# Kernel tuning notes

Hardware: AMD Instinct MI355X
Metric: run time of the kernel (lower is better)

## Reference

```python
import jax, jax.numpy as jnp
import numpy as np

W_WORKERS = 2
Q_LEN = 16
HIDDEN = 4096
N_HEADS = 32
N_KV = 8
HEAD_DIM = 128
L_SHARED = 8192
L_WORKER = 2048
THETA = 10000.0


def rotate_half(x):
    x1, x2 = jnp.split(x, 2, axis=-1)
    return jnp.concatenate((-x2, x1), axis=-1)


def rope_cos_sin(pos):
    # pos: int array [...]; returns cos,sin of shape [..., HEAD_DIM] (HF convention: freqs duplicated)
    inv = 1.0 / (THETA ** (jnp.arange(0, HEAD_DIM, 2, dtype=jnp.float32) / HEAD_DIM))
    ang = pos[..., None].astype(jnp.float32) * inv
    emb = jnp.concatenate((ang, ang), axis=-1)
    return jnp.cos(emb), jnp.sin(emb)


def setup_inputs() -> dict:
    key = jax.random.key(0)
    ks = jax.random.split(key, 16)
    std = 0.02
    # new keys are appended at positions L_WORKER..L_WORKER+Q-1 of each worker's own segment
    pos_new = jnp.broadcast_to(L_WORKER + jnp.arange(Q_LEN), (W_WORKERS, Q_LEN))
    cos_new, sin_new = rope_cos_sin(pos_new)
    return {
        'hidden_states': jax.random.normal(ks[0], (W_WORKERS, Q_LEN, HIDDEN), jnp.float32),
        'Wq': jax.random.normal(ks[1], (N_HEADS * HEAD_DIM, HIDDEN), jnp.float32) * std,
        'bq': jnp.zeros((N_HEADS * HEAD_DIM,), jnp.float32),
        'Wk': jax.random.normal(ks[2], (N_KV * HEAD_DIM, HIDDEN), jnp.float32) * std,
        'bk': jnp.zeros((N_KV * HEAD_DIM,), jnp.float32),
        'Wv': jax.random.normal(ks[3], (N_KV * HEAD_DIM, HIDDEN), jnp.float32) * std,
        'bv': jnp.zeros((N_KV * HEAD_DIM,), jnp.float32),
        'Wo': jax.random.normal(ks[4], (HIDDEN, N_HEADS * HEAD_DIM), jnp.float32) * std,
        'seg_shared_k': jax.random.normal(ks[5], (N_KV, L_SHARED, HEAD_DIM), jnp.float32),
        'seg_shared_v': jax.random.normal(ks[6], (N_KV, L_SHARED, HEAD_DIM), jnp.float32),
        'w0_k': jax.random.normal(ks[7], (N_KV, L_WORKER, HEAD_DIM), jnp.float32),
        'w0_v': jax.random.normal(ks[8], (N_KV, L_WORKER, HEAD_DIM), jnp.float32),
        'w1_k': jax.random.normal(ks[9], (N_KV, L_WORKER, HEAD_DIM), jnp.float32),
        'w1_v': jax.random.normal(ks[10], (N_KV, L_WORKER, HEAD_DIM), jnp.float32),
        'cos_new': cos_new,
        'sin_new': sin_new,
    }


def reference(hidden_states, Wq, bq, Wk, bk, Wv, bv, Wo,
              seg_shared_k, seg_shared_v, w0_k, w0_v, w1_k, w1_v,
              cos_new, sin_new):
    W, Q, _ = hidden_states.shape
    scale = HEAD_DIM ** -0.5
    # projections -> [W, n_heads, Q, D]
    q = (hidden_states @ Wq.T + bq).reshape(W, Q, N_HEADS, HEAD_DIM).transpose(0, 2, 1, 3)
    k_new = (hidden_states @ Wk.T + bk).reshape(W, Q, N_KV, HEAD_DIM).transpose(0, 2, 1, 3)
    v_new = (hidden_states @ Wv.T + bv).reshape(W, Q, N_KV, HEAD_DIM).transpose(0, 2, 1, 3)
    # rope new keys (unsqueeze_dim=1: broadcast over kv heads)
    c, s = cos_new[:, None], sin_new[:, None]
    k_new = k_new * c + rotate_half(k_new) * s
    # cache update: segment 0 = shared prompt, segment 1/2 = worker 0/1 own cache (grows by Q)
    keys = [seg_shared_k,
            jnp.concatenate([w0_k, k_new[0]], axis=1),
            jnp.concatenate([w1_k, k_new[1]], axis=1)]
    values = [seg_shared_v,
              jnp.concatenate([w0_v, v_new[0]], axis=1),
              jnp.concatenate([w1_v, v_new[1]], axis=1)]
    frag_lens = [L_SHARED, L_WORKER + Q, L_WORKER + Q]
    # worker w's view: [shared, other worker's cache, own cache]
    orders = [[0, 2, 1], [0, 1, 2]]
    loc = np.zeros((3, W_WORKERS, Q), dtype=np.int32)
    for w, order in enumerate(orders):
        pos = 0
        for seg in reversed(order):
            pos += frag_lens[seg]
            loc[seg, w] = np.arange(pos - Q, pos)
    loc = jnp.asarray(loc)  # [S, W, Q]
    cos_q, sin_q = rope_cos_sin(loc)  # [S, W, Q, D]
    # hogwild_rope: queries rotated per (segment, worker) location -> [S, W, H, Q, D]
    rq = q[None] * cos_q[:, :, None] + rotate_half(q)[None] * sin_q[:, :, None]
    rep = N_HEADS // N_KV
    scores, v_parts = [], []
    for seg in range(3):
        k_s = jnp.repeat(keys[seg], rep, axis=0)  # GQA expand [H, L_s, D]
        sc = jnp.einsum('whqd,hld->whql', rq[seg], k_s) * scale
        mask = jnp.arange(frag_lens[seg])[None, None, None, :] <= loc[seg][:, None, :, None]
        scores.append(jnp.where(mask, sc, jnp.finfo(sc.dtype).min))
        v_parts.append(jnp.repeat(values[seg], rep, axis=0))
    scores = jnp.concatenate(scores, axis=-1)        # [W, H, Q, Ltot] joint softmax over fragments
    probs = jax.nn.softmax(scores, axis=-1)
    v_all = jnp.concatenate(v_parts, axis=1)         # [H, Ltot, D]
    attn = jnp.einsum('whql,hld->whqd', probs, v_all)
    out = attn.transpose(0, 2, 1, 3).reshape(W, Q, N_HEADS * HEAD_DIM) @ Wo.T
    return out
```

## Files before the change

kernel.cpp:

```cpp
#include <hip/hip_runtime.h>
#include <hip/hip_fp16.h>
#include <cstdint>
#include <cstddef>

#define QL 16
#define LSH 8192
#define LWK 2048
#define SCALE 0.08838834764831845f

typedef __attribute__((ext_vector_type(8))) short short8;
typedef __attribute__((ext_vector_type(4))) short short4v;
typedef __attribute__((ext_vector_type(4))) float f32x4;
typedef __attribute__((ext_vector_type(8))) unsigned short ushort8v;

#if defined(__has_builtin)
#if __has_builtin(__builtin_amdgcn_mfma_f32_16x16x16bf16_1k)
#define HAVE_MFMA16 1
#endif
#endif

__device__ __forceinline__ unsigned short f2bf(float f) {
  unsigned int u = __float_as_uint(f);
  u += 0x7fffu + ((u >> 16) & 1u);
  return (unsigned short)(u >> 16);
}
__device__ __forceinline__ float bf2f(unsigned short b) {
  return __uint_as_float(((unsigned int)b) << 16);
}

__device__ __forceinline__ void gload_lds16(const float* g, float* lds) {
  __builtin_amdgcn_global_load_lds(
      (const __attribute__((address_space(1))) void*)g,
      (__attribute__((address_space(3))) void*)lds, 16, 0, 0);
}

__global__ __launch_bounds__(256) void k_cast(
    const float* __restrict__ in, unsigned short* __restrict__ outp, int n4)
{
  int i = blockIdx.x * 256 + threadIdx.x;
  if (i < n4) {
    float4 v = ((const float4*)in)[i];
    ushort4 p; p.x = f2bf(v.x); p.y = f2bf(v.y); p.z = f2bf(v.z); p.w = f2bf(v.w);
    ((ushort4*)outp)[i] = p;
  }
}

__global__ __launch_bounds__(256) void k_gemm4(
    const unsigned short* __restrict__ Xbf,
    const float* __restrict__ W0, const float* __restrict__ W1, const float* __restrict__ W2,
    const float* __restrict__ b0, const float* __restrict__ b1, const float* __restrict__ b2,
    float* __restrict__ outA, float* __restrict__ outB, int Ntot)
{
  __shared__ float Ws[16 * 516];
  const int bx = blockIdx.x;
  const int n0 = (bx >> 1) * 16;
  const int khalf = bx & 1;
  const float* W; const float* bias; int row0;
  if (n0 < 4096)      { W = W0; bias = b0; row0 = n0; }
  else if (n0 < 5120) { W = W1; bias = b1; row0 = n0 - 4096; }
  else                { W = W2; bias = b2; row0 = n0 - 5120; }
  const int t = threadIdx.x;
  const int w_id = t >> 6;
  const int lane = t & 63;
  const int l15 = lane & 15;
  const int quad = lane >> 4;
  const int cb0 = khalf * 2048;

  f32x4 C0 = {0.f,0.f,0.f,0.f}, C1 = {0.f,0.f,0.f,0.f};

  for (int c = 0; c < 4; ++c) {
    const int cbase = cb0 + c * 512;
    __syncthreads();
#pragma unroll
    for (int i = 0; i < 8; ++i) {
      int idx = w_id * 8 + i;
      int r = idx >> 1, hh = idx & 1;
      const float* g = W + (size_t)(row0 + r) * 4096 + cbase + hh * 256 + lane * 4;
      gload_lds16(g, &Ws[r * 516 + hh * 256]);
    }
    __syncthreads();
    const int wk = w_id * 128;
#pragma unroll
    for (int ks = 0; ks < 4; ++ks) {
      int ko = wk + ks * 32 + quad * 8;
      f32x4 wlo = *(const f32x4*)(&Ws[l15 * 516 + ko]);
      f32x4 whi = *(const f32x4*)(&Ws[l15 * 516 + ko + 4]);
      short8 bfr;
      bfr[0] = (short)f2bf(wlo[0]); bfr[1] = (short)f2bf(wlo[1]);
      bfr[2] = (short)f2bf(wlo[2]); bfr[3] = (short)f2bf(wlo[3]);
      bfr[4] = (short)f2bf(whi[0]); bfr[5] = (short)f2bf(whi[1]);
      bfr[6] = (short)f2bf(whi[2]); bfr[7] = (short)f2bf(whi[3]);
      short8 a0 = *(const short8*)(Xbf + (size_t)l15 * 4096 + cbase + ko);
      short8 a1 = *(const short8*)(Xbf + (size_t)(16 + l15) * 4096 + cbase + ko);
      C0 = __builtin_amdgcn_mfma_f32_16x16x32_bf16(a0, bfr, C0, 0, 0, 0);
      C1 = __builtin_amdgcn_mfma_f32_16x16x32_bf16(a1, bfr, C1, 0, 0, 0);
    }
  }
  __syncthreads();
  float* Red = Ws;
#pragma unroll
  for (int i = 0; i < 4; ++i) {
    Red[w_id * 512 + (quad * 4 + i) * 16 + l15] = C0[i];
    Red[w_id * 512 + 256 + (quad * 4 + i) * 16 + l15] = C1[i];
  }
  __syncthreads();
  float* dst = khalf ? outB : outA;
#pragma unroll
  for (int e = t; e < 512; e += 256) {
    float s = Red[e] + Red[512 + e] + Red[1024 + e] + Red[1536 + e];
    int m = e >> 4, n = e & 15;
    if (khalf == 0 && bias) s += bias[row0 + n];
    dst[(size_t)m * Ntot + n0 + n] = s;
  }
}

__global__ __launch_bounds__(256) void k_add(
    const float* __restrict__ A, const float* __restrict__ B,
    float* __restrict__ o, int n4)
{
  int i = blockIdx.x * 256 + threadIdx.x;
  if (i < n4) {
    float4 a = ((const float4*)A)[i], b = ((const float4*)B)[i];
    float4 r; r.x = a.x + b.x; r.y = a.y + b.y; r.z = a.z + b.z; r.w = a.w + b.w;
    ((float4*)o)[i] = r;
  }
}

__global__ __launch_bounds__(256) void k_rope(
    const float* __restrict__ qA, const float* __restrict__ qB,
    const float* __restrict__ cosn, const float* __restrict__ sinn,
    unsigned short* __restrict__ rq, unsigned short* __restrict__ knew,
    unsigned short* __restrict__ vnew)
{
  const int g = blockIdx.x * 256 + threadIdx.x;
  const float LOGTH = 9.210340371976184f;
  if (g < 393216) {
    int d = g & 127, q = (g >> 7) & 15, head = (g >> 11) & 31, w = (g >> 16) & 1, var = g >> 17;
    int tok = w * 16 + q;
    int col = head * 128 + d;
    size_t ix = (size_t)tok * 6144 + col;
    float val = qA[ix] + qB[ix];
    size_t ir = (d < 64) ? ix + 64 : ix - 64;
    float rot = qA[ir] + qB[ir];
    if (d < 64) rot = -rot;
    int pos = (var == 0 ? 12304 : (var == 1 ? 4112 : 2048)) + q;
    int i = d & 63;
    float inv = expf(-(float)i * (LOGTH / 64.0f));
    float ang = (float)pos * inv;
    float c = cosf(ang), s = sinf(ang);
    rq[g] = f2bf((val * c + rot * s) * SCALE);
  } else {
    int g2 = g - 393216;
    if (g2 < 65536) {
      int isv = (g2 >= 32768);
      if (isv) g2 -= 32768;
      int d = g2 & 127, q = (g2 >> 7) & 15, h = (g2 >> 11) & 7, w = (g2 >> 14) & 1;
      int tok = w * 16 + q;
      if (isv) {
        size_t ix = (size_t)tok * 6144 + 5120 + h * 128 + d;
        vnew[g2] = f2bf(qA[ix] + qB[ix]);
      } else {
        size_t ix = (size_t)tok * 6144 + 4096 + h * 128 + d;
        float val = qA[ix] + qB[ix];
        size_t ir = (d < 64) ? ix + 64 : ix - 64;
        float rot = qA[ir] + qB[ir];
        if (d < 64) rot = -rot;
        float c = cosn[tok * 128 + d], s = sinn[tok * 128 + d];
        knew[g2] = f2bf(val * c + rot * s);
      }
    }
  }
}

__global__ __launch_bounds__(512, 2) void k_attn(
    const float* __restrict__ shk, const float* __restrict__ shv,
    const float* __restrict__ w0k, const float* __restrict__ w0v,
    const float* __restrict__ w1k, const float* __restrict__ w1v,
    const unsigned short* __restrict__ rq,
    const unsigned short* __restrict__ knew, const unsigned short* __restrict__ vnew,
    __half* __restrict__ accP, float* __restrict__ lP)
{
  __shared__ alignas(16) unsigned short Ks[64 * 136];
  __shared__ alignas(16) unsigned short Vts[128 * 72];
#ifndef HAVE_MFMA16
  __shared__ alignas(16) unsigned short Plds[8 * 16 * 72];
#endif

  const int h = blockIdx.x / 50;
  const int cidx = blockIdx.x % 50;
  int kind, k0, nk; bool is_new;
  if (cidx < 32)      { kind = 0; k0 = cidx * 256; nk = 256; is_new = false; }
  else if (cidx < 41) { int c = cidx - 32; kind = 1; k0 = c * 256; nk = (c == 8) ? 16 : 256; is_new = (c == 8); }
  else                { int c = cidx - 41; kind = 2; k0 = c * 256; nk = (c == 8) ? 16 : 256; is_new = (c == 8); }

  const int t = threadIdx.x;
  const int w_id = t >> 6;
  const int lane = t & 63;
  const int l15 = lane & 15;
  const int quad = lane >> 4;
  const int worker = w_id >> 2;
  const int hq = w_id & 3;
  const int col4 = t & 31;
  const int rowb = t >> 5;
  const int dv = t & 127;
  const int tg = t >> 7;

  int var; bool causal;
  if (kind == 0)      { var = 0; causal = false; }
  else if (kind == 1) { var = (worker == 0) ? 2 : 1; causal = (worker == 0); }
  else                { var = (worker == 1) ? 2 : 1; causal = (worker == 1); }

  const float* Ksrc = (kind == 0) ? (shk + (size_t)h * LSH * 128)
                     : (kind == 1) ? (w0k + (size_t)h * LWK * 128)
                                   : (w1k + (size_t)h * LWK * 128);
  const float* Vsrc = (kind == 0) ? (shv + (size_t)h * LSH * 128)
                     : (kind == 1) ? (w0v + (size_t)h * LWK * 128)
                                   : (w1v + (size_t)h * LWK * 128);
  const int wseg = (kind == 2) ? 1 : 0;
  const unsigned short* knsrc = knew + ((size_t)wseg * 8 + h) * 16 * 128;
  const unsigned short* vnsrc = vnew + ((size_t)wseg * 8 + h) * 16 * 128;

  const int head = h * 4 + hq;
  short8 arq[4];
  {
    const unsigned short* base =
        rq + ((((size_t)var * 2 + worker) * 32 + head) * 16 + l15) * 128 + quad * 8;
#pragma unroll
    for (int ks = 0; ks < 4; ++ks) arq[ks] = *(const short8*)(base + ks * 32);
  }

  float lrow = 0.f;
  f32x4 acc[8];
#pragma unroll
  for (int dt = 0; dt < 8; ++dt) acc[dt] = {0.f,0.f,0.f,0.f};

  float4 kf[4];
  float  vf[16];

  auto load_tile = [&](int st) {
    const int kb = k0 + st * 64;
    if (!is_new) {
#pragma unroll
      for (int i = 0; i < 4; ++i)
        kf[i] = *(const float4*)(Ksrc + (size_t)(kb + i * 16 + rowb) * 128 + col4 * 4);
#pragma unroll
      for (int g = 0; g < 2; ++g)
#pragma unroll
        for (int i = 0; i < 8; ++i)
          vf[g * 8 + i] = Vsrc[(size_t)(kb + g * 32 + tg * 8 + i) * 128 + dv];
    } else {
#pragma unroll
      for (int i = 0; i < 4; ++i) {
        ushort4 p = *(const ushort4*)(knsrc + (size_t)((i * 16 + rowb) & 15) * 128 + col4 * 4);
        kf[i].x = bf2f(p.x); kf[i].y = bf2f(p.y);
        kf[i].z = bf2f(p.z); kf[i].w = bf2f(p.w);
      }
#pragma unroll
      for (int g = 0; g < 2; ++g)
#pragma unroll
        for (int i = 0; i < 8; ++i)
          vf[g * 8 + i] = bf2f(vnsrc[(size_t)((g * 32 + tg * 8 + i) & 15) * 128 + dv]);
    }
  };

  const int nst = (nk + 63) >> 6;
  load_tile(0);

  for (int st = 0; st < nst; ++st) {
    __syncthreads();
#pragma unroll
    for (int i = 0; i < 4; ++i) {
      ushort4 p; p.x = f2bf(kf[i].x); p.y = f2bf(kf[i].y);
      p.z = f2bf(kf[i].z); p.w = f2bf(kf[i].w);
      *(ushort4*)(&Ks[(i * 16 + rowb) * 136 + col4 * 4]) = p;
    }
#pragma unroll
    for (int g = 0; g < 2; ++g) {
      ushort8v p;
#pragma unroll
      for (int i = 0; i < 8; ++i) p[i] = f2bf(vf[g * 8 + i]);
      *(ushort8v*)(&Vts[dv * 72 + (g * 4 + tg) * 8]) = p;
    }
    __syncthreads();
    if (st + 1 < nst) load_tile(st + 1);

    f32x4 S[4];
#pragma unroll
    for (int nt = 0; nt < 4; ++nt) S[nt] = {0.f,0.f,0.f,0.f};
#pragma unroll
    for (int ks = 0; ks < 4; ++ks)
#pragma unroll
      for (int nt = 0; nt < 4; ++nt) {
        short8 kfr = *(const short8*)(&Ks[(nt * 16 + l15) * 136 + ks * 32 + quad * 8]);
        S[nt] = __builtin_amdgcn_mfma_f32_16x16x32_bf16(kfr, arq[ks], S[nt], 0, 0, 0);
      }
    if (is_new) {
#pragma unroll
      for (int nt = 0; nt < 4; ++nt)
#pragma unroll
        for (int i = 0; i < 4; ++i) {
          int loc = st * 64 + nt * 16 + quad * 4 + i;
          if (loc >= nk || (causal && loc > l15)) S[nt][i] = -3.0e38f;
        }
    }
    float rs = 0.0f;
#pragma unroll
    for (int nt = 0; nt < 4; ++nt)
#pragma unroll
      for (int i = 0; i < 4; ++i) {
        float p = __expf(fminf(S[nt][i], 60.0f));
        S[nt][i] = p;
        rs += p;
      }
#ifdef HAVE_MFMA16
    short4v pv[4];
#pragma unroll
    for (int nt = 0; nt < 4; ++nt) {
      short4v pp;
      pp[0] = (short)f2bf(S[nt][0]); pp[1] = (short)f2bf(S[nt][1]);
      pp[2] = (short)f2bf(S[nt][2]); pp[3] = (short)f2bf(S[nt][3]);
      pv[nt] = pp;
    }
#else
#pragma unroll
    for (int nt = 0; nt < 4; ++nt)
#pragma unroll
      for (int i = 0; i < 4; ++i)
        Plds[w_id * (16 * 72) + l15 * 72 + nt * 16 + quad * 4 + i] = f2bf(S[nt][i]);
#endif
    rs += __shfl_xor(rs, 16, 64);
    rs += __shfl_xor(rs, 32, 64);
    lrow += rs;

#ifdef HAVE_MFMA16
#pragma unroll
    for (int dt = 0; dt < 8; ++dt)
#pragma unroll
      for (int kc = 0; kc < 4; ++kc) {
        short4v vfr = *(const short4v*)(&Vts[(dt * 16 + l15) * 72 + kc * 16 + quad * 4]);
        acc[dt] = __builtin_amdgcn_mfma_f32_16x16x16bf16_1k(pv[kc], vfr, acc[dt], 0, 0, 0);
      }
#else
    short8 ap[2];
#pragma unroll
    for (int ks2 = 0; ks2 < 2; ++ks2)
      ap[ks2] = *(const short8*)(
          &Plds[w_id * (16 * 72) + l15 * 72 + ks2 * 32 + quad * 8]);
#pragma unroll
    for (int dt = 0; dt < 8; ++dt)
#pragma unroll
      for (int ks2 = 0; ks2 < 2; ++ks2) {
        short8 vfr = *(const short8*)(&Vts[(dt * 16 + l15) * 72 + ks2 * 32 + quad * 8]);
        acc[dt] = __builtin_amdgcn_mfma_f32_16x16x32_bf16(ap[ks2], vfr, acc[dt], 0, 0, 0);
      }
#endif
  }

  __half* accB = accP + (size_t)blockIdx.x * 128 * 128;
  const int wrow = worker * 64 + hq * 16;
#pragma unroll
  for (int dt = 0; dt < 8; ++dt)
#pragma unroll
    for (int i = 0; i < 4; ++i) {
      int row = wrow + quad * 4 + i;
      int d = dt * 16 + l15;
      accB[row * 128 + d] = __float2half(acc[dt][i]);
    }
  if (quad == 0) {
    int row = wrow + l15;
    lP[(size_t)blockIdx.x * 128 + row] = lrow;
  }
}

__global__ __launch_bounds__(128) void k_combine(
    const __half* __restrict__ accP, const float* __restrict__ lP,
    unsigned short* __restrict__ attnX)
{
  __shared__ float sl[50];
  const int h = blockIdx.x >> 7;
  const int r = blockIdx.x & 127;
  const int d = threadIdx.x;
  if (d < 50) sl[d] = lP[(size_t)(h * 50 + d) * 128 + r];
  __syncthreads();
  float L = 0.0f, A = 0.0f;
#pragma unroll
  for (int c = 0; c < 50; ++c) L += sl[c];
#pragma unroll
  for (int cc = 0; cc < 50; cc += 10) {
    float p[10];
#pragma unroll
    for (int i = 0; i < 10; ++i)
      p[i] = __half2float(accP[((size_t)(h * 50 + cc + i) * 128 + r) * 128 + d]);
#pragma unroll
    for (int i = 0; i < 10; ++i) A += p[i];
  }
  int workerv = r >> 6, headpairv = (r >> 5) & 1, mtv = (r >> 4) & 1, q = r & 15;
  int head = h * 4 + headpairv * 2 + mtv;
  attnX[(size_t)(workerv * 16 + q) * 4096 + head * 128 + d] = f2bf(A / L);
}

extern "C" void kernel_launch(void* const* d_in, const int* in_sizes, int n_in,
                              void* d_out, int out_size, void* d_ws, size_t ws_size,
                              hipStream_t stream)
{
  const float* hs   = (const float*)d_in[0];
  const float* Wq   = (const float*)d_in[1];
  const float* bq   = (const float*)d_in[2];
  const float* Wk   = (const float*)d_in[3];
  const float* bk   = (const float*)d_in[4];
  const float* Wv   = (const float*)d_in[5];
  const float* bv   = (const float*)d_in[6];
  const float* Wo   = (const float*)d_in[7];
  const float* shk  = (const float*)d_in[8];
  const float* shv  = (const float*)d_in[9];
  const float* w0k  = (const float*)d_in[10];
  const float* w0v  = (const float*)d_in[11];
  const float* w1k  = (const float*)d_in[12];
  const float* w1v  = (const float*)d_in[13];
  const float* cosn = (const float*)d_in[14];
  const float* sinn = (const float*)d_in[15];
  float* out = (float*)d_out;

  char* ws = (char*)d_ws;
  float*          qkvA   = (float*)(ws + 0);
  unsigned short* rq     = (unsigned short*)(ws + 786432);
  unsigned short* knew   = (unsigned short*)(ws + 1572864);
  unsigned short* vnew   = (unsigned short*)(ws + 1638400);
  unsigned short* hsbf   = (unsigned short*)(ws + 1703936);
  unsigned short* attnXb = (unsigned short*)(ws + 1966080);
  float*          lP     = (float*)(ws + 2228224);
  __half*         accP   = (__half*)(ws + 2433024);
  float*          qkvB   = (float*)(ws + 15540224);
  float*          outA   = (float*)(ws + 2433024);
  float*          outB   = (float*)(ws + 2433024 + 786432);

  k_cast<<<128, 256, 0, stream>>>(hs, hsbf, 32768);
  k_gemm4<<<768, 256, 0, stream>>>(hsbf, Wq, Wk, Wv, bq, bk, bv, qkvA, qkvB, 6144);
  k_rope<<<1792, 256, 0, stream>>>(qkvA, qkvB, cosn, sinn, rq, knew, vnew);
  k_attn<<<400, 512, 0, stream>>>(shk, shv, w0k, w0v, w1k, w1v, rq, knew, vnew, accP, lP);
  k_combine<<<1024, 128, 0, stream>>>(accP, lP, attnXb);
  k_gemm4<<<512, 256, 0, stream>>>(attnXb, Wo, Wo, Wo, nullptr, nullptr, nullptr, outA, outB, 4096);
  k_add<<<192, 256, 0, stream>>>(outA, outB, out, 49152);
}
```

Measured before the change: 296.8 us.

## Double-buffer LDS tiles in QKV GEMM and attention with explicit waitcnt pipelining

The QKV projection GEMM now double-buffers its weight tile in LDS. It prefetches the next chunk with global_load_lds while computing the current one, and loads the bf16 activations into registers ahead of time. The attention kernel also double-buffers its K/V LDS tiles, issues the next tile's global loads through inline asm, and replaces one of the two per-iteration __syncthreads with manual waitcnt plus s_barrier. The aim is to overlap global memory latency with MFMA work and cut barrier stalls. The cost is doubled LDS use, which may lower occupancy in k_attn (512 threads, 2 blocks per SM), and manual vmcnt accounting that is fragile.

```diff
diff --git a/kernel.cpp b/kernel.cpp
--- a/kernel.cpp
+++ b/kernel.cpp
@@ -34,6 +34,22 @@
       (__attribute__((address_space(3))) void*)lds, 16, 0, 0);
 }
 
+__device__ __forceinline__ void gload_f4(float4& d, const float* p) {
+  asm volatile("global_load_dwordx4 %0, %1, off"
+               : "=v"(d)
+               : "v"((const __attribute__((address_space(1))) float*)p));
+}
+__device__ __forceinline__ void gload_f1(float& d, const float* p) {
+  asm volatile("global_load_dword %0, %1, off"
+               : "=v"(d)
+               : "v"((const __attribute__((address_space(1))) float*)p));
+}
+__device__ __forceinline__ void gload_s8(short8& d, const unsigned short* p) {
+  asm volatile("global_load_dwordx4 %0, %1, off"
+               : "=v"(d)
+               : "v"((const __attribute__((address_space(1))) unsigned short*)p));
+}
+
 __global__ __launch_bounds__(256) void k_cast(
     const float* __restrict__ in, unsigned short* __restrict__ outp, int n4)
 {
@@ -51,7 +67,7 @@
     const float* __restrict__ b0, const float* __restrict__ b1, const float* __restrict__ b2,
     float* __restrict__ outA, float* __restrict__ outB, int Ntot)
 {
-  __shared__ float Ws[16 * 516];
+  __shared__ float Ws[2][16 * 516];
   const int bx = blockIdx.x;
   const int n0 = (bx >> 1) * 16;
   const int khalf = bx & 1;
@@ -65,39 +81,61 @@
   const int l15 = lane & 15;
   const int quad = lane >> 4;
   const int cb0 = khalf * 2048;
+  const int wk = w_id * 128;
 
   f32x4 C0 = {0.f,0.f,0.f,0.f}, C1 = {0.f,0.f,0.f,0.f};
-
-  for (int c = 0; c < 4; ++c) {
+  short8 xa0[4], xa1[4];
+
+  auto stage = [&](int c, int b) {
     const int cbase = cb0 + c * 512;
-    __syncthreads();
 #pragma unroll
     for (int i = 0; i < 8; ++i) {
       int idx = w_id * 8 + i;
       int r = idx >> 1, hh = idx & 1;
       const float* g = W + (size_t)(row0 + r) * 4096 + cbase + hh * 256 + lane * 4;
-      gload_lds16(g, &Ws[r * 516 + hh * 256]);
-    }
-    __syncthreads();
-    const int wk = w_id * 128;
+      gload_lds16(g, &Ws[b][r * 516 + hh * 256]);
+    }
+  };
+
+  stage(0, 0);
+#pragma unroll
+  for (int c = 0; c < 4; ++c) {
+    const int cbase = cb0 + c * 512;
 #pragma unroll
     for (int ks = 0; ks < 4; ++ks) {
       int ko = wk + ks * 32 + quad * 8;
-      f32x4 wlo = *(const f32x4*)(&Ws[l15 * 516 + ko]);
-      f32x4 whi = *(const f32x4*)(&Ws[l15 * 516 + ko + 4]);
+      gload_s8(xa0[ks], Xbf + (size_t)l15 * 4096 + cbase + ko);
+      gload_s8(xa1[ks], Xbf + (size_t)(16 + l15) * 4096 + cbase + ko);
+    }
+    __builtin_amdgcn_sched_barrier(0);
+    if (c < 3) {
+      stage(c + 1, (c + 1) & 1);
+      asm volatile("s_waitcnt vmcnt(8)" ::: "memory");
+    } else {
+      asm volatile("s_waitcnt vmcnt(0)" ::: "memory");
+    }
+    __builtin_amdgcn_sched_barrier(0);
+    __builtin_amdgcn_s_barrier();
+    __builtin_amdgcn_sched_barrier(0);
+    const float* Wsb = Ws[c & 1];
+#pragma unroll
+    for (int ks = 0; ks < 4; ++ks) {
+      int ko = wk + ks * 32 + quad * 8;
+      f32x4 wlo = *(const f32x4*)(&Wsb[l15 * 516 + ko]);
+      f32x4 whi = *(const f32x4*)(&Wsb[l15 * 516 + ko + 4]);
       short8 bfr;
       bfr[0] = (short)f2bf(wlo[0]); bfr[1] = (short)f2bf(wlo[1]);
       bfr[2] = (short)f2bf(wlo[2]); bfr[3] = (short)f2bf(wlo[3]);
       bfr[4] = (short)f2bf(whi[0]); bfr[5] = (short)f2bf(whi[1]);
       bfr[6] = (short)f2bf(whi[2]); bfr[7] = (short)f2bf(whi[3]);
-      short8 a0 = *(const short8*)(Xbf + (size_t)l15 * 4096 + cbase + ko);
-      short8 a1 = *(const short8*)(Xbf + (size_t)(16 + l15) * 4096 + cbase + ko);
-      C0 = __builtin_amdgcn_mfma_f32_16x16x32_bf16(a0, bfr, C0, 0, 0, 0);
-      C1 = __builtin_amdgcn_mfma_f32_16x16x32_bf16(a1, bfr, C1, 0, 0, 0);
-    }
-  }
-  __syncthreads();
-  float* Red = Ws;
+      C0 = __builtin_amdgcn_mfma_f32_16x16x32_bf16(xa0[ks], bfr, C0, 0, 0, 0);
+      C1 = __builtin_amdgcn_mfma_f32_16x16x32_bf16(xa1[ks], bfr, C1, 0, 0, 0);
+    }
+    __builtin_amdgcn_sched_barrier(0);
+    __builtin_amdgcn_s_barrier();
+    __builtin_amdgcn_sched_barrier(0);
+  }
+  float* Red = &Ws[0][0];
 #pragma unroll
   for (int i = 0; i < 4; ++i) {
     Red[w_id * 512 + (quad * 4 + i) * 16 + l15] = C0[i];
@@ -180,8 +218,8 @@
     const unsigned short* __restrict__ knew, const unsigned short* __restrict__ vnew,
     __half* __restrict__ accP, float* __restrict__ lP)
 {
-  __shared__ alignas(16) unsigned short Ks[64 * 136];
-  __shared__ alignas(16) unsigned short Vts[128 * 72];
+  __shared__ alignas(16) unsigned short Ks[2][64 * 136];
+  __shared__ alignas(16) unsigned short Vts[2][128 * 72];
 #ifndef HAVE_MFMA16
   __shared__ alignas(16) unsigned short Plds[8 * 16 * 72];
 #endif
@@ -237,52 +275,60 @@
   float4 kf[4];
   float  vf[16];
 
-  auto load_tile = [&](int st) {
-    const int kb = k0 + st * 64;
-    if (!is_new) {
-#pragma unroll
-      for (int i = 0; i < 4; ++i)
-        kf[i] = *(const float4*)(Ksrc + (size_t)(kb + i * 16 + rowb) * 128 + col4 * 4);
-#pragma unroll
-      for (int g = 0; g < 2; ++g)
-#pragma unroll
-        for (int i = 0; i < 8; ++i)
-          vf[g * 8 + i] = Vsrc[(size_t)(kb + g * 32 + tg * 8 + i) * 128 + dv];
-    } else {
-#pragma unroll
-      for (int i = 0; i < 4; ++i) {
-        ushort4 p = *(const ushort4*)(knsrc + (size_t)((i * 16 + rowb) & 15) * 128 + col4 * 4);
-        kf[i].x = bf2f(p.x); kf[i].y = bf2f(p.y);
-        kf[i].z = bf2f(p.z); kf[i].w = bf2f(p.w);
-      }
-#pragma unroll
-      for (int g = 0; g < 2; ++g)
-#pragma unroll
-        for (int i = 0; i < 8; ++i)
-          vf[g * 8 + i] = bf2f(vnsrc[(size_t)((g * 32 + tg * 8 + i) & 15) * 128 + dv]);
-    }
+  const float* kbase = Ksrc + (size_t)(k0 + rowb) * 128 + col4 * 4;
+  const float* vbase = Vsrc + (size_t)(k0 + tg * 8) * 128 + dv;
+
+  auto issue_tile = [&](int st) {
+    const float* kp = kbase + (size_t)st * 64 * 128;
+#pragma unroll
+    for (int i = 0; i < 4; ++i) gload_f4(kf[i], kp + (size_t)i * 16 * 128);
+    const float* vp = vbase + (size_t)st * 64 * 128;
+#pragma unroll
+    for (int g = 0; g < 2; ++g)
+#pragma unroll
+      for (int i = 0; i < 8; ++i)
+        gload_f1(vf[g * 8 + i], vp + (size_t)(g * 32 + i) * 128);
   };
 
   const int nst = (nk + 63) >> 6;
-  load_tile(0);
+  if (!is_new) {
+    issue_tile(0);
+  } else {
+#pragma unroll
+    for (int i = 0; i < 4; ++i) {
+      ushort4 p = *(const ushort4*)(knsrc + (size_t)((i * 16 + rowb) & 15) * 128 + col4 * 4);
+      kf[i].x = bf2f(p.x); kf[i].y = bf2f(p.y);
+      kf[i].z = bf2f(p.z); kf[i].w = bf2f(p.w);
+    }
+#pragma unroll
+    for (int g = 0; g < 2; ++g)
+#pragma unroll
+      for (int i = 0; i < 8; ++i)
+        vf[g * 8 + i] = bf2f(vnsrc[(size_t)((g * 32 + tg * 8 + i) & 15) * 128 + dv]);
+  }
 
   for (int st = 0; st < nst; ++st) {
-    __syncthreads();
+    const int pb = st & 1;
+    asm volatile("s_waitcnt vmcnt(0)" ::: "memory");
+    __builtin_amdgcn_sched_barrier(0);
 #pragma unroll
     for (int i = 0; i < 4; ++i) {
       ushort4 p; p.x = f2bf(kf[i].x); p.y = f2bf(kf[i].y);
       p.z = f2bf(kf[i].z); p.w = f2bf(kf[i].w);
-      *(ushort4*)(&Ks[(i * 16 + rowb) * 136 + col4 * 4]) = p;
+      *(ushort4*)(&Ks[pb][(i * 16 + rowb) * 136 + col4 * 4]) = p;
     }
 #pragma unroll
     for (int g = 0; g < 2; ++g) {
       ushort8v p;
 #pragma unroll
       for (int i = 0; i < 8; ++i) p[i] = f2bf(vf[g * 8 + i]);
-      *(ushort8v*)(&Vts[dv * 72 + (g * 4 + tg) * 8]) = p;
-    }
-    __syncthreads();
-    if (st + 1 < nst) load_tile(st + 1);
+      *(ushort8v*)(&Vts[pb][dv * 72 + (g * 4 + tg) * 8]) = p;
+    }
+    if (st + 1 < nst) issue_tile(st + 1);
+    asm volatile("s_waitcnt lgkmcnt(0)" ::: "memory");
+    __builtin_amdgcn_sched_barrier(0);
+    __builtin_amdgcn_s_barrier();
+    __builtin_amdgcn_sched_barrier(0);
 
     f32x4 S[4];
 #pragma unroll
@@ -291,7 +337,7 @@
     for (int ks = 0; ks < 4; ++ks)
 #pragma unroll
       for (int nt = 0; nt < 4; ++nt) {
-        short8 kfr = *(const short8*)(&Ks[(nt * 16 + l15) * 136 + ks * 32 + quad * 8]);
+        short8 kfr = *(const short8*)(&Ks[pb][(nt * 16 + l15) * 136 + ks * 32 + quad * 8]);
         S[nt] = __builtin_amdgcn_mfma_f32_16x16x32_bf16(kfr, arq[ks], S[nt], 0, 0, 0);
       }
     if (is_new) {
@@ -337,7 +383,7 @@
     for (int dt = 0; dt < 8; ++dt)
 #pragma unroll
       for (int kc = 0; kc < 4; ++kc) {
-        short4v vfr = *(const short4v*)(&Vts[(dt * 16 + l15) * 72 + kc * 16 + quad * 4]);
+        short4v vfr = *(const short4v*)(&Vts[pb][(dt * 16 + l15) * 72 + kc * 16 + quad * 4]);
         acc[dt] = __builtin_amdgcn_mfma_f32_16x16x16bf16_1k(pv[kc], vfr, acc[dt], 0, 0, 0);
       }
 #else
@@ -350,7 +396,7 @@
     for (int dt = 0; dt < 8; ++dt)
 #pragma unroll
       for (int ks2 = 0; ks2 < 2; ++ks2) {
-        short8 vfr = *(const short8*)(&Vts[(dt * 16 + l15) * 72 + ks2 * 32 + quad * 8]);
+        short8 vfr = *(const short8*)(&Vts[pb][(dt * 16 + l15) * 72 + ks2 * 32 + quad * 8]);
         acc[dt] = __builtin_amdgcn_mfma_f32_16x16x32_bf16(ap[ks2], vfr, acc[dt], 0, 0, 0);
       }
 #endif
```

New measurement: 295.4 us. No clear change (-0.5%).
